# Optimization experiments

Measured on AMD Instinct MI355X. Metric: run time of the kernel, lower is better.

Reference implementation:

```python
import jax, jax.numpy as jnp
import numpy as np


def setup_inputs() -> dict:
    key = jax.random.key(0)
    k1, k2, k3 = jax.random.split(key, 3)
    num_paths, horizon, d_obs = 1024, 64, 64
    d_input = int(d_obs + d_obs * (d_obs + 1) / 2 + 1)  # 2145
    observations = jax.random.normal(k1, (num_paths, horizon, d_obs), dtype=jnp.float32)
    weights = jax.random.normal(k2, (horizon, d_input), dtype=jnp.float32)
    biases = jax.random.normal(k3, (horizon,), dtype=jnp.float32)
    return {"observations": observations, "weights": weights, "biases": biases}


def reference(observations, weights, biases):
    # observations: [N, H, D]; weights: [H, D + D*(D+1)/2 + 1]; biases: [H]
    d_obs = observations.shape[-1]
    iu, ju = jnp.triu_indices(d_obs)  # upper-triangular (i <= j) pairs, matching the torch loop order
    quad = observations[..., iu] * observations[..., ju]      # [N, H, D*(D+1)/2]
    feats = jnp.concatenate([observations, quad], axis=-1)    # [N, H, d_input-1]
    # The torch code leaves the last feature column as zero, so weights[:, -1]
    # contributes nothing; slice it off instead of materializing a zero column.
    values = jnp.einsum("nhd,hd->nh", feats, weights[:, :-1]) + biases
    return values
```

## Files before the change

### kernel.cpp

```cpp
#include <hip/hip_runtime.h>


#define DOBS 64
#define NH   64
#define WROW 2145
#define KAUG 96
#define LSTR 104

typedef unsigned short u16;
typedef __attribute__((ext_vector_type(8))) short short8;
typedef __attribute__((ext_vector_type(4))) short short4v;
typedef __attribute__((ext_vector_type(4))) float floatx4;

__device__ __forceinline__ u16 f2bf(float f) {
    unsigned u = __float_as_uint(f);
    return (u16)((u + 0x7FFF + ((u >> 16) & 1)) >> 16);
}
__device__ __forceinline__ float bf2f(u16 b) {
    return __uint_as_float(((unsigned)b) << 16);
}

__global__ __launch_bounds__(256) void qvf_main(
    const float* __restrict__ obs, const float* __restrict__ weights,
    const float* __restrict__ biases, float* __restrict__ out, int N)
{
    __shared__ u16 O16[DOBS * LSTR];
    __shared__ u16 W16[DOBS * LSTR];

    const int h    = blockIdx.x & (NH - 1);
    const int tidx = blockIdx.x >> 6;
    const int lane = threadIdx.x & 63;
    const int wv   = threadIdx.x >> 6;
    const int n0   = tidx * 64;

    {
        const float* __restrict__ wsrc = weights + h * WROW;
#pragma unroll
        for (int p = 0; p < 3; ++p) {
            const int s   = p * 256 + threadIdx.x;
            const int i   = s / 12;
            const int seg = s - i * 12;
            const int j0  = seg * 8;
            const int qb  = DOBS + i * DOBS - (i * (i - 1)) / 2 - i;
            short8 v8;
#pragma unroll
            for (int e = 0; e < 8; ++e) {
                const int j = j0 + e;
                float v = 0.f;
                if (j < DOBS) {
                    if (j >= i) v = wsrc[qb + j];
                } else if (j == DOBS) {
                    v = wsrc[i];
                }
                v8[e] = (short)f2bf(v);
            }
            *(short8*)&W16[i * LSTR + j0] = v8;
        }
    }

    {
        const float* __restrict__ src = obs + ((size_t)n0 * NH + h) * DOBS;
#pragma unroll
        for (int p = 0; p < 4; ++p) {
            const int g  = p * 256 + threadIdx.x;
            const int r  = g >> 4;
            const int c4 = g & 15;
            const floatx4 v = *(const floatx4*)(src + (size_t)r * (NH * DOBS) + c4 * 4);
            short4v sv;
            sv[0] = (short)f2bf(v.x); sv[1] = (short)f2bf(v.y);
            sv[2] = (short)f2bf(v.z); sv[3] = (short)f2bf(v.w);
            *(short4v*)&O16[r * LSTR + c4 * 4] = sv;
        }
        const int r   = threadIdx.x >> 2;
        const int seg = threadIdx.x & 3;
        short8 z = (short8)0;
        if (seg == 0) z[0] = (short)0x3F80;
        *(short8*)&O16[r * LSTR + DOBS + seg * 8] = z;
    }
    __syncthreads();

    floatx4 acc[4];
#pragma unroll
    for (int ct = 0; ct < 4; ++ct) acc[ct] = (floatx4)0.f;

    const int mrow = wv * 16 + (lane & 15);
    const int q    = lane >> 4;
#pragma unroll
    for (int ks = 0; ks < 3; ++ks) {
        const short8 a = *(const short8*)&O16[mrow * LSTR + ks * 32 + q * 8];
#pragma unroll
        for (int ct = 0; ct < 4; ++ct) {
            const int i = ct * 16 + (lane & 15);
            const short8 b = *(const short8*)&W16[i * LSTR + ks * 32 + q * 8];
            acc[ct] = __builtin_amdgcn_mfma_f32_16x16x32_bf16(a, b, acc[ct], 0, 0, 0);
        }
    }

    float P[4] = {0.f, 0.f, 0.f, 0.f};
    const int col = lane & 15;
#pragma unroll
    for (int ct = 0; ct < 4; ++ct) {
#pragma unroll
        for (int r = 0; r < 4; ++r) {
            const int row = wv * 16 + q * 4 + r;
            const u16 ov = O16[row * LSTR + ct * 16 + col];
            P[r] = fmaf(acc[ct][r], bf2f(ov), P[r]);
        }
    }
#pragma unroll
    for (int msk = 1; msk < 16; msk <<= 1) {
#pragma unroll
        for (int r = 0; r < 4; ++r) P[r] += __shfl_xor(P[r], msk, 64);
    }
    if (col == 0) {
        const float b = biases[h];
#pragma unroll
        for (int r = 0; r < 4; ++r) {
            const int row = wv * 16 + q * 4 + r;
            out[(size_t)(n0 + row) * NH + h] = P[r] + b;
        }
    }
}

extern "C" void kernel_launch(void* const* d_in, const int* in_sizes, int n_in,
                              void* d_out, int out_size, void* d_ws, size_t ws_size,
                              hipStream_t stream) {
    const float* obs     = (const float*)d_in[0];
    const float* weights = (const float*)d_in[1];
    const float* biases  = (const float*)d_in[2];
    float* out           = (float*)d_out;

    const int N = in_sizes[0] / (NH * DOBS);
    qvf_main<<<dim3((N / 64) * NH), dim3(256), 0, stream>>>(obs, weights, biases, out, N);
}
```

Baseline: 69.72 us.

## Load quadratic weights coalesced, scatter into triangular LDS, fold linear term into accumulator

Weight staging now reads the packed upper-triangular weight row with fully coalesced loads into registers, then scatters each element to its (i,j) slot in LDS using a sqrt-based inverse triangular index. The old per-thread gather with branches and strided reads is replaced. The linear weights are moved out of the augmented K dimension: they initialise the MFMA accumulators, so K drops from 96 to 64 and one MFMA step per tile is removed. This costs an extra barrier, scattered 16-bit LDS stores that may hit bank conflicts, and a float sqrt per element.

```diff
diff --git a/kernel.cpp b/kernel.cpp
--- a/kernel.cpp
+++ b/kernel.cpp
@@ -4,8 +4,8 @@
 #define DOBS 64
 #define NH   64
 #define WROW 2145
-#define KAUG 96
-#define LSTR 104
+#define NQUAD 2080
+#define LSTR 72
 
 typedef unsigned short u16;
 typedef __attribute__((ext_vector_type(8))) short short8;
@@ -19,6 +19,9 @@
 __device__ __forceinline__ float bf2f(u16 b) {
     return __uint_as_float(((unsigned)b) << 16);
 }
+__device__ __forceinline__ int tri_start(int i) {
+    return (i * (129 - i)) >> 1;
+}
 
 __global__ __launch_bounds__(256) void qvf_main(
     const float* __restrict__ obs, const float* __restrict__ weights,
@@ -26,6 +29,7 @@
 {
     __shared__ u16 O16[DOBS * LSTR];
     __shared__ u16 W16[DOBS * LSTR];
+    __shared__ float LW[DOBS];
 
     const int h    = blockIdx.x & (NH - 1);
     const int tidx = blockIdx.x >> 6;
@@ -33,29 +37,23 @@
     const int wv   = threadIdx.x >> 6;
     const int n0   = tidx * 64;
 
+    const float* __restrict__ wsrc = weights + h * WROW;
+
+    float wq[8];
+#pragma unroll
+    for (int p = 0; p < 8; ++p)
+        wq[p] = wsrc[DOBS + p * 256 + threadIdx.x];
+    float wq8 = 0.f;
+    if (threadIdx.x < NQUAD - 2048)
+        wq8 = wsrc[DOBS + 2048 + threadIdx.x];
+
+    if (threadIdx.x < DOBS) LW[threadIdx.x] = wsrc[threadIdx.x];
+
     {
-        const float* __restrict__ wsrc = weights + h * WROW;
-#pragma unroll
-        for (int p = 0; p < 3; ++p) {
-            const int s   = p * 256 + threadIdx.x;
-            const int i   = s / 12;
-            const int seg = s - i * 12;
-            const int j0  = seg * 8;
-            const int qb  = DOBS + i * DOBS - (i * (i - 1)) / 2 - i;
-            short8 v8;
-#pragma unroll
-            for (int e = 0; e < 8; ++e) {
-                const int j = j0 + e;
-                float v = 0.f;
-                if (j < DOBS) {
-                    if (j >= i) v = wsrc[qb + j];
-                } else if (j == DOBS) {
-                    v = wsrc[i];
-                }
-                v8[e] = (short)f2bf(v);
-            }
-            *(short8*)&W16[i * LSTR + j0] = v8;
-        }
+        const short8 z = (short8)0;
+        *(short8*)&W16[threadIdx.x * 8]         = z;
+        *(short8*)&W16[(256 + threadIdx.x) * 8] = z;
+        if (threadIdx.x < 64) *(short8*)&W16[(512 + threadIdx.x) * 8] = z;
     }
 
     {
@@ -71,38 +69,51 @@
             sv[2] = (short)f2bf(v.z); sv[3] = (short)f2bf(v.w);
             *(short4v*)&O16[r * LSTR + c4 * 4] = sv;
         }
-        const int r   = threadIdx.x >> 2;
-        const int seg = threadIdx.x & 3;
-        short8 z = (short8)0;
-        if (seg == 0) z[0] = (short)0x3F80;
-        *(short8*)&O16[r * LSTR + DOBS + seg * 8] = z;
     }
     __syncthreads();
 
+#pragma unroll
+    for (int p = 0; p < 9; ++p) {
+        const int q = p * 256 + threadIdx.x;
+        if (p == 8 && q >= NQUAD) break;
+        const float v = (p < 8) ? wq[p] : wq8;
+        const int   t = 16641 - 8 * q;
+        int i = (int)((129.0f - __builtin_sqrtf((float)t)) * 0.5f);
+        i = (i < 0) ? 0 : ((i > 63) ? 63 : i);
+        if (q < tri_start(i)) --i;
+        if (q >= tri_start(i + 1)) ++i;
+        const int j = i + (q - tri_start(i));
+        W16[i * LSTR + j] = f2bf(v);
+    }
+    __syncthreads();
+
+    const int col = lane & 15;
+    const int qq  = lane >> 4;
     floatx4 acc[4];
 #pragma unroll
-    for (int ct = 0; ct < 4; ++ct) acc[ct] = (floatx4)0.f;
+    for (int ct = 0; ct < 4; ++ct) {
+        const float wl = LW[ct * 16 + col];
+        acc[ct][0] = wl; acc[ct][1] = wl; acc[ct][2] = wl; acc[ct][3] = wl;
+    }
 
-    const int mrow = wv * 16 + (lane & 15);
-    const int q    = lane >> 4;
+    const int mrow = wv * 16 + col;
 #pragma unroll
-    for (int ks = 0; ks < 3; ++ks) {
-        const short8 a = *(const short8*)&O16[mrow * LSTR + ks * 32 + q * 8];
+    for (int ks = 0; ks < 2; ++ks) {
+        const short8 a = *(const short8*)&O16[mrow * LSTR + ks * 32 + qq * 8];
 #pragma unroll
         for (int ct = 0; ct < 4; ++ct) {
-            const int i = ct * 16 + (lane & 15);
-            const short8 b = *(const short8*)&W16[i * LSTR + ks * 32 + q * 8];
+            const int i = ct * 16 + col;
+            const short8 b = *(const short8*)&W16[i * LSTR + ks * 32 + qq * 8];
             acc[ct] = __builtin_amdgcn_mfma_f32_16x16x32_bf16(a, b, acc[ct], 0, 0, 0);
         }
     }
 
     float P[4] = {0.f, 0.f, 0.f, 0.f};
-    const int col = lane & 15;
 #pragma unroll
     for (int ct = 0; ct < 4; ++ct) {
 #pragma unroll
         for (int r = 0; r < 4; ++r) {
-            const int row = wv * 16 + q * 4 + r;
+            const int row = wv * 16 + qq * 4 + r;
             const u16 ov = O16[row * LSTR + ct * 16 + col];
             P[r] = fmaf(acc[ct][r], bf2f(ov), P[r]);
         }
@@ -116,7 +127,7 @@
         const float b = biases[h];
 #pragma unroll
         for (int r = 0; r < 4; ++r) {
-            const int row = wv * 16 + q * 4 + r;
+            const int row = wv * 16 + qq * 4 + r;
             out[(size_t)(n0 + row) * NH + h] = P[r] + b;
         }
     }
```

Measured after the change: 68.33 us. 1.02x faster.
